# Kernel optimization log

Measured on AMD Instinct MI355X. Metric: run time of the kernel, lower is better.

The kernel has to match this reference:

```python
import jax, jax.numpy as jnp
import numpy as np

N_NODES = 50000
N_EDGES = 800000
LATENT = 32
NODE_IN = 6
EDGE_IN = 3
STEPS = 10
OUT_DIM = 1
NEG_SLOPE = 0.01
LN_EPS = 1e-5


def _leaky(x):
    return jnp.where(x >= 0, x, NEG_SLOPE * x)


def _layernorm(x, scale, bias):
    mu = jnp.mean(x, axis=-1, keepdims=True)
    var = jnp.mean(jnp.square(x - mu), axis=-1, keepdims=True)
    return (x - mu) * jax.lax.rsqrt(var + LN_EPS) * scale + bias


def setup_inputs() -> dict:
    key = jax.random.key(0)
    ks = jax.random.split(key, 24)
    g = lambda i, shape, fan_in: (jax.random.normal(ks[i], shape, jnp.float32)
                                  / np.sqrt(fan_in)).astype(jnp.float32)
    return {
        "x": jax.random.normal(ks[0], (N_NODES, NODE_IN), jnp.float32),
        "edge_attr": jax.random.normal(ks[1], (N_EDGES, EDGE_IN), jnp.float32),
        "senders": jax.random.randint(ks[2], (N_EDGES,), 0, N_NODES, jnp.int32),
        "receivers": jax.random.randint(ks[3], (N_EDGES,), 0, N_NODES, jnp.int32),
        # input embedders (Linear + LeakyReLU)
        "node_enc_W": g(4, (NODE_IN, LATENT), NODE_IN),
        "node_enc_b": jnp.zeros((LATENT,), jnp.float32),
        "edge_enc_W": g(5, (EDGE_IN, LATENT), EDGE_IN),
        "edge_enc_b": jnp.zeros((LATENT,), jnp.float32),
        # per-step edge update: concat(e, x_src, x_dst) -> latent
        "edge_W": g(6, (STEPS, 3 * LATENT, LATENT), 3 * LATENT),
        "edge_b": jnp.zeros((STEPS, LATENT), jnp.float32),
        "edge_ln_scale": jnp.ones((STEPS, LATENT), jnp.float32),
        "edge_ln_bias": jnp.zeros((STEPS, LATENT), jnp.float32),
        # per-step node update: concat(x, agg) -> latent
        "node_W": g(7, (STEPS, 2 * LATENT, LATENT), 2 * LATENT),
        "node_b": jnp.zeros((STEPS, LATENT), jnp.float32),
        "node_ln_scale": jnp.ones((STEPS, LATENT), jnp.float32),
        "node_ln_bias": jnp.zeros((STEPS, LATENT), jnp.float32),
        # decoder
        "dec_W1": g(8, (LATENT, LATENT), LATENT),
        "dec_b1": jnp.zeros((LATENT,), jnp.float32),
        "dec_W2": g(9, (LATENT, OUT_DIM), LATENT),
        "dec_b2": jnp.zeros((OUT_DIM,), jnp.float32),
    }


def _forward(x, edge_attr, senders, receivers,
             node_enc_W, node_enc_b, edge_enc_W, edge_enc_b,
             edge_W, edge_b, edge_ln_scale, edge_ln_bias,
             node_W, node_b, node_ln_scale, node_ln_bias,
             dec_W1, dec_b1, dec_W2, dec_b2):
    n = x.shape[0]
    # encode raw features into latent space
    h = _leaky(x @ node_enc_W + node_enc_b)            # [N, L]
    e = _leaky(edge_attr @ edge_enc_W + edge_enc_b)    # [E, L]
    # receiver in-degree for scatter-mean (constant across steps)
    cnt = jax.ops.segment_sum(jnp.ones((e.shape[0],), e.dtype), receivers,
                              num_segments=n)
    inv_cnt = (1.0 / jnp.maximum(cnt, 1.0))[:, None]   # [N, 1]

    def step(carry, p):
        h, e = carry
        eW, eb, es, ebi, nW, nb, ns, nbi = p
        # edge update: MLP(concat(e, h_src, h_dst)) + inner LN + residual
        m = jnp.concatenate([e, h[senders], h[receivers]], axis=-1)  # [E, 3L]
        m = _layernorm(_leaky(m @ eW + eb), es, ebi)
        e = e + m
        # node update: scatter-mean over receivers, MLP + inner LN + residual
        agg = jax.ops.segment_sum(e, receivers, num_segments=n) * inv_cnt
        u = jnp.concatenate([h, agg], axis=-1)                       # [N, 2L]
        u = _layernorm(_leaky(u @ nW + nb), ns, nbi)
        h = h + u
        return (h, e), None

    (h, e), _ = jax.lax.scan(step, (h, e),
                             (edge_W, edge_b, edge_ln_scale, edge_ln_bias,
                              node_W, node_b, node_ln_scale, node_ln_bias))
    # decoder: Linear -> LeakyReLU -> Linear
    return _leaky(h @ dec_W1 + dec_b1) @ dec_W2 + dec_b2  # [N, 1]


def reference(x, edge_attr, senders, receivers,
              node_enc_W, node_enc_b, edge_enc_W, edge_enc_b,
              edge_W, edge_b, edge_ln_scale, edge_ln_bias,
              node_W, node_b, node_ln_scale, node_ln_bias,
              dec_W1, dec_b1, dec_W2, dec_b2):
    return _forward(x, edge_attr, senders, receivers,
                    node_enc_W, node_enc_b, edge_enc_W, edge_enc_b,
                    edge_W, edge_b, edge_ln_scale, edge_ln_bias,
                    node_W, node_b, node_ln_scale, node_ln_bias,
                    dec_W1, dec_b1, dec_W2, dec_b2)
```

## Files before the change

kernel.cpp:

```cpp
#include <hip/hip_runtime.h>
#include <hip/hip_bf16.h>

#define N_NODES 50000
#define N_EDGES 800000
#define LATENT 32
#define STEPS 10
#define NEG_SLOPE 0.01f
#define LN_EPS 1e-5f
#define N_TILES (N_EDGES / 16)
#define TPW 4
#define TILES_PER_BLOCK 16
#define SCAN_BLK 256
#define SCAN_NBLK ((N_NODES + SCAN_BLK - 1) / SCAN_BLK)
#define STG_STRIDE 36

typedef __attribute__((ext_vector_type(8))) __bf16 bf16x8;
typedef __attribute__((ext_vector_type(4))) __bf16 bf16x4;
typedef __attribute__((ext_vector_type(4))) float f32x4;

__device__ __forceinline__ float leaky(float x) {
    return x >= 0.0f ? x : NEG_SLOPE * x;
}

__device__ __forceinline__ float4 f4fma(float a, float4 b, float4 c) {
    c.x += a * b.x; c.y += a * b.y; c.z += a * b.z; c.w += a * b.w;
    return c;
}

__device__ __forceinline__ bf16x4 pack4(float4 v) {
    bf16x4 o;
    o[0] = (__bf16)v.x; o[1] = (__bf16)v.y; o[2] = (__bf16)v.z; o[3] = (__bf16)v.w;
    return o;
}


__global__ void encode_nodes_kernel(const float* __restrict__ x,
                                    const float* __restrict__ W,
                                    const float* __restrict__ b,
                                    float* __restrict__ h,
                                    __bf16* __restrict__ hbf) {
    __shared__ __align__(16) float Ws[6 * 32];
    __shared__ __align__(16) float bs[32];
    int tid = threadIdx.x;
    if (tid < 192) Ws[tid] = W[tid];
    if (tid < 32) bs[tid] = b[tid];
    __syncthreads();
    int n = blockIdx.x * blockDim.x + tid;
    if (n >= N_NODES) return;
    float xv[6];
#pragma unroll
    for (int k = 0; k < 6; k++) xv[k] = x[(size_t)n * 6 + k];
    float4 acc[8];
#pragma unroll
    for (int q = 0; q < 8; q++) acc[q] = *(const float4*)&bs[q * 4];
#pragma unroll
    for (int k = 0; k < 6; k++) {
#pragma unroll
        for (int q = 0; q < 8; q++) {
            float4 w = *(const float4*)&Ws[k * 32 + q * 4];
            acc[q] = f4fma(xv[k], w, acc[q]);
        }
    }
#pragma unroll
    for (int q = 0; q < 8; q++) {
        float4 o = acc[q];
        o.x = leaky(o.x); o.y = leaky(o.y); o.z = leaky(o.z); o.w = leaky(o.w);
        *(float4*)&h[(size_t)n * 32 + q * 4] = o;
        *(bf16x4*)&hbf[(size_t)n * 32 + q * 4] = pack4(o);
    }
}


__global__ void count_kernel(const int* __restrict__ recv, int* __restrict__ cnt) {
    int i = blockIdx.x * blockDim.x + threadIdx.x;
    if (i < N_EDGES) atomicAdd(&cnt[recv[i]], 1);
}

__global__ void csr_reduce_kernel(const int* __restrict__ cnt, int* __restrict__ partial) {
    __shared__ int sdata[SCAN_BLK];
    int tid = threadIdx.x;
    int idx = blockIdx.x * SCAN_BLK + tid;
    sdata[tid] = (idx < N_NODES) ? cnt[idx] : 0;
    __syncthreads();
#pragma unroll
    for (int off = SCAN_BLK / 2; off > 0; off >>= 1) {
        if (tid < off) sdata[tid] += sdata[tid + off];
        __syncthreads();
    }
    if (tid == 0) partial[blockIdx.x] = sdata[0];
}

__global__ void csr_scan_partials_kernel(int* __restrict__ partial,
                                         int* __restrict__ row_start) {
    __shared__ int sdata[SCAN_BLK];
    int tid = threadIdx.x;
    int v = (tid < SCAN_NBLK) ? partial[tid] : 0;
    sdata[tid] = v;
    __syncthreads();
#pragma unroll
    for (int off = 1; off < SCAN_BLK; off <<= 1) {
        int t = (tid >= off) ? sdata[tid - off] : 0;
        __syncthreads();
        sdata[tid] += t;
        __syncthreads();
    }
    if (tid < SCAN_NBLK) partial[tid] = sdata[tid] - v;
    if (tid == SCAN_BLK - 1) row_start[N_NODES] = sdata[SCAN_BLK - 1];
}

__global__ void csr_apply_kernel(const int* __restrict__ cnt,
                                 const int* __restrict__ partial,
                                 int* __restrict__ row_start,
                                 int* __restrict__ cursor) {
    __shared__ int sdata[SCAN_BLK];
    int tid = threadIdx.x;
    int idx = blockIdx.x * SCAN_BLK + tid;
    int v = (idx < N_NODES) ? cnt[idx] : 0;
    sdata[tid] = v;
    __syncthreads();
#pragma unroll
    for (int off = 1; off < SCAN_BLK; off <<= 1) {
        int t = (tid >= off) ? sdata[tid - off] : 0;
        __syncthreads();
        sdata[tid] += t;
        __syncthreads();
    }
    if (idx < N_NODES) {
        int out = partial[blockIdx.x] + sdata[tid] - v;
        row_start[idx] = out;
        cursor[idx] = out;
    }
}

__global__ void scatter_encode_kernel(const float* __restrict__ ea,
                                      const int* __restrict__ senders,
                                      const int* __restrict__ receivers,
                                      int* __restrict__ cursor,
                                      const float* __restrict__ W,
                                      const float* __restrict__ b,
                                      __bf16* __restrict__ e,
                                      unsigned int* __restrict__ sr_p) {
    __shared__ __align__(16) float Ws[3 * 32];
    __shared__ __align__(16) float bs[32];
    int tid = threadIdx.x;
    if (tid < 96) Ws[tid] = W[tid];
    if (tid < 32) bs[tid] = b[tid];
    __syncthreads();
    int i = blockIdx.x * blockDim.x + tid;
    if (i >= N_EDGES) return;
    int s = senders[i];
    int r = receivers[i];
    float xv[3];
#pragma unroll
    for (int k = 0; k < 3; k++) xv[k] = ea[(size_t)i * 3 + k];
    int pos = atomicAdd(&cursor[r], 1);
    float4 acc[8];
#pragma unroll
    for (int q = 0; q < 8; q++) acc[q] = *(const float4*)&bs[q * 4];
#pragma unroll
    for (int k = 0; k < 3; k++) {
#pragma unroll
        for (int q = 0; q < 8; q++) {
            float4 w = *(const float4*)&Ws[k * 32 + q * 4];
            acc[q] = f4fma(xv[k], w, acc[q]);
        }
    }
    __bf16* er = e + (size_t)pos * 32;
#pragma unroll
    for (int q = 0; q < 4; q++) {
        float4 lo = acc[2 * q], hi = acc[2 * q + 1];
        bf16x8 v;
        v[0] = (__bf16)leaky(lo.x); v[1] = (__bf16)leaky(lo.y);
        v[2] = (__bf16)leaky(lo.z); v[3] = (__bf16)leaky(lo.w);
        v[4] = (__bf16)leaky(hi.x); v[5] = (__bf16)leaky(hi.y);
        v[6] = (__bf16)leaky(hi.z); v[7] = (__bf16)leaky(hi.w);
        *(bf16x8*)(er + q * 8) = v;
    }
    sr_p[pos] = (unsigned int)s | ((unsigned int)r << 16);
}


__global__ __launch_bounds__(256) void edge_mfma_kernel(
    __bf16* __restrict__ e,
    const __bf16* __restrict__ hbf,
    const unsigned int* __restrict__ srp,
    const float* __restrict__ W,
    const float* __restrict__ bias,
    const float* __restrict__ ln_s,
    const float* __restrict__ ln_b) {
    __shared__ __align__(16) float stg[4][16 * STG_STRIDE];
    int tid = threadIdx.x;

    const int wave = tid >> 6;
    const int lane = tid & 63;
    const int n_ = lane & 15;
    const int quad = lane >> 4;
    const int rr = lane >> 2;
    const int jj = lane & 3;

    bf16x8 bf[3][2];
#pragma unroll
    for (int kc = 0; kc < 3; kc++)
#pragma unroll
        for (int oh = 0; oh < 2; oh++) {
            bf16x8 f;
#pragma unroll
            for (int j = 0; j < 8; j++)
                f[j] = (__bf16)W[(kc * 32 + quad * 8 + j) * 32 + oh * 16 + n_];
            bf[kc][oh] = f;
        }
    float bia0 = bias[n_], bia1 = bias[16 + n_];
    float lns8[8], lnb8[8];
    {
        f32x4 sa = *(const f32x4*)&ln_s[jj * 8];
        f32x4 sb = *(const f32x4*)&ln_s[jj * 8 + 4];
        f32x4 ba = *(const f32x4*)&ln_b[jj * 8];
        f32x4 bb = *(const f32x4*)&ln_b[jj * 8 + 4];
#pragma unroll
        for (int i = 0; i < 4; i++) {
            lns8[i] = sa[i]; lns8[4 + i] = sb[i];
            lnb8[i] = ba[i]; lnb8[4 + i] = bb[i];
        }
    }

    int tile0 = blockIdx.x * TILES_PER_BLOCK + wave * TPW;
    int ntiles = min(TPW, N_TILES - tile0);
    if (ntiles <= 0) return;
    float* mystg = stg[wave];
    const int ed0 = tile0 * 16 + n_;

    unsigned int sr0 = srp[ed0];
    bf16x8 aE = *(const bf16x8*)&e[(size_t)ed0 * 32 + quad * 8];
    bf16x8 aS = *(const bf16x8*)&hbf[(size_t)(sr0 & 0xFFFFu) * 32 + quad * 8];
    bf16x8 aR = *(const bf16x8*)&hbf[(size_t)(sr0 >> 16) * 32 + quad * 8];
    bf16x8 old = *(const bf16x8*)&e[(size_t)(tile0 * 16 + rr) * 32 + jj * 8];
    unsigned int sr_n = 0;
    if (ntiles > 1) sr_n = srp[ed0 + 16];

    for (int t = 0; t < ntiles; t++) {
        int e0 = (tile0 + t) * 16;

        f32x4 acc[2] = {{0.f, 0.f, 0.f, 0.f}, {0.f, 0.f, 0.f, 0.f}};
#pragma unroll
        for (int oh = 0; oh < 2; oh++) {
            acc[oh] = __builtin_amdgcn_mfma_f32_16x16x32_bf16(aE, bf[0][oh], acc[oh], 0, 0, 0);
            acc[oh] = __builtin_amdgcn_mfma_f32_16x16x32_bf16(aS, bf[1][oh], acc[oh], 0, 0, 0);
            acc[oh] = __builtin_amdgcn_mfma_f32_16x16x32_bf16(aR, bf[2][oh], acc[oh], 0, 0, 0);
        }

        bf16x8 aE_n = aE, aS_n = aS, aR_n = aR, old_n = old;
        if (t + 1 < ntiles) {
            int edn = ed0 + (t + 1) * 16;
            aE_n = *(const bf16x8*)&e[(size_t)edn * 32 + quad * 8];
            aS_n = *(const bf16x8*)&hbf[(size_t)(sr_n & 0xFFFFu) * 32 + quad * 8];
            aR_n = *(const bf16x8*)&hbf[(size_t)(sr_n >> 16) * 32 + quad * 8];
            old_n = *(const bf16x8*)&e[(size_t)(e0 + 16 + rr) * 32 + jj * 8];
            if (t + 2 < ntiles) sr_n = srp[ed0 + (t + 2) * 16];
        }

#pragma unroll
        for (int oh = 0; oh < 2; oh++)
#pragma unroll
            for (int g = 0; g < 4; g++)
                mystg[(quad * 4 + g) * STG_STRIDE + oh * 16 + n_] =
                    leaky(acc[oh][g] + (oh ? bia1 : bia0));
        __builtin_amdgcn_wave_barrier();

        f32x4 va = *(const f32x4*)&mystg[rr * STG_STRIDE + jj * 8];
        f32x4 vb = *(const f32x4*)&mystg[rr * STG_STRIDE + jj * 8 + 4];
        float s1 = va[0] + va[1] + va[2] + va[3] + vb[0] + vb[1] + vb[2] + vb[3];
        float s2 = va[0]*va[0] + va[1]*va[1] + va[2]*va[2] + va[3]*va[3]
                 + vb[0]*vb[0] + vb[1]*vb[1] + vb[2]*vb[2] + vb[3]*vb[3];
        s1 += __shfl_xor(s1, 1);  s2 += __shfl_xor(s2, 1);
        s1 += __shfl_xor(s1, 2);  s2 += __shfl_xor(s2, 2);
        float mu = s1 * (1.0f / 32.0f);
        float var = s2 * (1.0f / 32.0f) - mu * mu;
        float inv = rsqrtf(fmaxf(var, 0.0f) + LN_EPS);

        float v[8] = {va[0], va[1], va[2], va[3], vb[0], vb[1], vb[2], vb[3]};
        bf16x8 outp;
#pragma unroll
        for (int i = 0; i < 8; i++)
            outp[i] = (__bf16)((float)old[i] + (v[i] - mu) * inv * lns8[i] + lnb8[i]);
        *(bf16x8*)&e[(size_t)(e0 + rr) * 32 + jj * 8] = outp;
        __builtin_amdgcn_wave_barrier();

        aE = aE_n; aS = aS_n; aR = aR_n; old = old_n;
    }
}


__global__ __launch_bounds__(256, 1) void node_kernel(
                            float* __restrict__ h,
                            __bf16* __restrict__ hbf,
                            const __bf16* __restrict__ e,
                            const int* __restrict__ row_start,
                            const float* __restrict__ W,
                            const float* __restrict__ bias,
                            const float* __restrict__ ln_s,
                            const float* __restrict__ ln_b) {
    __shared__ __align__(16) float Ws[64 * 32];
    __shared__ __align__(16) float prm[96];
    int tid = threadIdx.x;
    {
        const float4* Wg = (const float4*)W;
        float4* Wl = (float4*)Ws;
#pragma unroll
        for (int r = 0; r < 2; r++) Wl[tid + r * 256] = Wg[tid + r * 256];
        if (tid < 32) {
            prm[tid] = bias[tid];
            prm[32 + tid] = ln_s[tid];
            prm[64 + tid] = ln_b[tid];
        }
    }
    __syncthreads();
    int n = blockIdx.x * blockDim.x + tid;
    if (n >= N_NODES) return;

    int beg = row_start[n], end = row_start[n + 1];
    float c[64];
#pragma unroll
    for (int q = 0; q < 8; q++) {
        float4 v = *(const float4*)&h[(size_t)n * 32 + q * 4];
        c[q * 4 + 0] = v.x; c[q * 4 + 1] = v.y; c[q * 4 + 2] = v.z; c[q * 4 + 3] = v.w;
    }
    float s[32];
#pragma unroll
    for (int k = 0; k < 32; k++) s[k] = 0.0f;

    int j = beg;
    for (; j + 3 < end; j += 4) {
        bf16x8 v[16];
#pragma unroll
        for (int r = 0; r < 4; r++) {
            const __bf16* er = e + (size_t)(j + r) * 32;
#pragma unroll
            for (int q = 0; q < 4; q++) v[r * 4 + q] = *(const bf16x8*)(er + q * 8);
        }
#pragma unroll
        for (int r = 0; r < 4; r++)
#pragma unroll
            for (int q = 0; q < 4; q++)
#pragma unroll
                for (int k = 0; k < 8; k++)
                    s[q * 8 + k] += (float)v[r * 4 + q][k];
    }
    for (; j < end; j++) {
        const __bf16* er = e + (size_t)j * 32;
#pragma unroll
        for (int q = 0; q < 4; q++) {
            bf16x8 v = *(const bf16x8*)(er + q * 8);
#pragma unroll
            for (int k = 0; k < 8; k++) s[q * 8 + k] += (float)v[k];
        }
    }
    float ic = 1.0f / fmaxf((float)(end - beg), 1.0f);
#pragma unroll
    for (int k = 0; k < 32; k++) c[32 + k] = s[k] * ic;

    float4 acc[8];
#pragma unroll
    for (int q = 0; q < 8; q++) acc[q] = *(const float4*)&prm[q * 4];
#pragma unroll
    for (int k = 0; k < 64; k++) {
#pragma unroll
        for (int q = 0; q < 8; q++) {
            float4 w = *(const float4*)&Ws[k * 32 + q * 4];
            acc[q] = f4fma(c[k], w, acc[q]);
        }
    }
    float m[32];
#pragma unroll
    for (int q = 0; q < 8; q++) {
        m[q * 4 + 0] = leaky(acc[q].x);
        m[q * 4 + 1] = leaky(acc[q].y);
        m[q * 4 + 2] = leaky(acc[q].z);
        m[q * 4 + 3] = leaky(acc[q].w);
    }
    float s1 = 0.0f, s2 = 0.0f;
#pragma unroll
    for (int i = 0; i < 32; i++) { s1 += m[i]; s2 += m[i] * m[i]; }
    float mu = s1 * (1.0f / 32.0f);
    float var = s2 * (1.0f / 32.0f) - mu * mu;
    float inv = rsqrtf(fmaxf(var, 0.0f) + LN_EPS);
#pragma unroll
    for (int q = 0; q < 8; q++) {
        float4 sc = *(const float4*)&prm[32 + q * 4];
        float4 bi = *(const float4*)&prm[64 + q * 4];
        float4 res;
        res.x = c[q * 4 + 0] + (m[q * 4 + 0] - mu) * inv * sc.x + bi.x;
        res.y = c[q * 4 + 1] + (m[q * 4 + 1] - mu) * inv * sc.y + bi.y;
        res.z = c[q * 4 + 2] + (m[q * 4 + 2] - mu) * inv * sc.z + bi.z;
        res.w = c[q * 4 + 3] + (m[q * 4 + 3] - mu) * inv * sc.w + bi.w;
        *(float4*)&h[(size_t)n * 32 + q * 4] = res;
        *(bf16x4*)&hbf[(size_t)n * 32 + q * 4] = pack4(res);
    }
}


__global__ void decoder_kernel(const float* __restrict__ h,
                               const float* __restrict__ W1,
                               const float* __restrict__ b1,
                               const float* __restrict__ W2,
                               const float* __restrict__ b2,
                               float* __restrict__ out) {
    __shared__ __align__(16) float W1s[32 * 32];
    __shared__ __align__(16) float prm[65];
    int tid = threadIdx.x;
    {
        const float4* Wg = (const float4*)W1;
        float4* Wl = (float4*)W1s;
        Wl[tid] = Wg[tid];
        if (tid < 32) { prm[tid] = b1[tid]; prm[32 + tid] = W2[tid]; }
        if (tid == 0) prm[64] = b2[0];
    }
    __syncthreads();
    int n = blockIdx.x * blockDim.x + tid;
    if (n >= N_NODES) return;
    float hv[32];
#pragma unroll
    for (int q = 0; q < 8; q++) {
        float4 v = *(const float4*)&h[(size_t)n * 32 + q * 4];
        hv[q * 4 + 0] = v.x; hv[q * 4 + 1] = v.y; hv[q * 4 + 2] = v.z; hv[q * 4 + 3] = v.w;
    }
    float4 acc[8];
#pragma unroll
    for (int q = 0; q < 8; q++) acc[q] = *(const float4*)&prm[q * 4];
#pragma unroll
    for (int k = 0; k < 32; k++) {
#pragma unroll
        for (int q = 0; q < 8; q++) {
            float4 w = *(const float4*)&W1s[k * 32 + q * 4];
            acc[q] = f4fma(hv[k], w, acc[q]);
        }
    }
    float o = prm[64];
#pragma unroll
    for (int q = 0; q < 8; q++) {
        o += leaky(acc[q].x) * prm[32 + q * 4 + 0];
        o += leaky(acc[q].y) * prm[32 + q * 4 + 1];
        o += leaky(acc[q].z) * prm[32 + q * 4 + 2];
        o += leaky(acc[q].w) * prm[32 + q * 4 + 3];
    }
    out[n] = o;
}


extern "C" void kernel_launch(void* const* d_in, const int* in_sizes, int n_in,
                              void* d_out, int out_size, void* d_ws, size_t ws_size,
                              hipStream_t stream) {
    const float* x          = (const float*)d_in[0];
    const float* edge_attr  = (const float*)d_in[1];
    const int*   senders    = (const int*)d_in[2];
    const int*   receivers  = (const int*)d_in[3];
    const float* node_enc_W = (const float*)d_in[4];
    const float* node_enc_b = (const float*)d_in[5];
    const float* edge_enc_W = (const float*)d_in[6];
    const float* edge_enc_b = (const float*)d_in[7];
    const float* edge_W     = (const float*)d_in[8];
    const float* edge_b     = (const float*)d_in[9];
    const float* edge_ln_s  = (const float*)d_in[10];
    const float* edge_ln_b  = (const float*)d_in[11];
    const float* node_W     = (const float*)d_in[12];
    const float* node_b     = (const float*)d_in[13];
    const float* node_ln_s  = (const float*)d_in[14];
    const float* node_ln_b  = (const float*)d_in[15];
    const float* dec_W1     = (const float*)d_in[16];
    const float* dec_b1     = (const float*)d_in[17];
    const float* dec_W2     = (const float*)d_in[18];
    const float* dec_b2     = (const float*)d_in[19];
    float* out = (float*)d_out;

    char* ws = (char*)d_ws;
    size_t off = 0;
    auto alloc = [&](size_t bytes) -> void* {
        void* p = ws + off;
        off = (off + bytes + 255) & ~(size_t)255;
        return p;
    };
    float*        h         = (float*)alloc((size_t)N_NODES * 32 * 4);
    __bf16*       hbf       = (__bf16*)alloc((size_t)N_NODES * 32 * 2);
    __bf16*       e         = (__bf16*)alloc((size_t)N_EDGES * 32 * 2);
    int*          cnt       = (int*)alloc((size_t)N_NODES * 4);
    int*          row_start = (int*)alloc((size_t)(N_NODES + 1) * 4);
    int*          cursor    = (int*)alloc((size_t)N_NODES * 4);
    unsigned int* sr_p      = (unsigned int*)alloc((size_t)N_EDGES * 4);
    int*          partial   = (int*)alloc((size_t)SCAN_BLK * 4);
    (void)ws_size; (void)in_sizes; (void)n_in; (void)out_size;

    hipMemsetAsync(cnt, 0, (size_t)N_NODES * 4, stream);
    encode_nodes_kernel<<<(N_NODES + 255) / 256, 256, 0, stream>>>(x, node_enc_W, node_enc_b, h, hbf);
    count_kernel<<<(N_EDGES + 255) / 256, 256, 0, stream>>>(receivers, cnt);
    csr_reduce_kernel<<<SCAN_NBLK, SCAN_BLK, 0, stream>>>(cnt, partial);
    csr_scan_partials_kernel<<<1, SCAN_BLK, 0, stream>>>(partial, row_start);
    csr_apply_kernel<<<SCAN_NBLK, SCAN_BLK, 0, stream>>>(cnt, partial, row_start, cursor);
    scatter_encode_kernel<<<(N_EDGES + 255) / 256, 256, 0, stream>>>(
        edge_attr, senders, receivers, cursor, edge_enc_W, edge_enc_b, e, sr_p);

    int edge_blocks = (N_TILES + TILES_PER_BLOCK - 1) / TILES_PER_BLOCK;
    for (int s = 0; s < STEPS; s++) {
        edge_mfma_kernel<<<edge_blocks, 256, 0, stream>>>(
            e, hbf, sr_p,
            edge_W + (size_t)s * 96 * 32, edge_b + s * 32,
            edge_ln_s + s * 32, edge_ln_b + s * 32);
        node_kernel<<<(N_NODES + 255) / 256, 256, 0, stream>>>(
            h, hbf, e, row_start, node_W + (size_t)s * 64 * 32, node_b + s * 32,
            node_ln_s + s * 32, node_ln_b + s * 32);
    }
    decoder_kernel<<<(N_NODES + 255) / 256, 256, 0, stream>>>(h, dec_W1, dec_b1, dec_W2, dec_b2, out);
}
```

Before: 681.7 us.

## Fuse edge and node updates into one per-step kernel over receiver-sorted node blocks

Each message-passing step now runs as one kernel instead of separate edge and node kernels. A block owns 64 consecutive nodes and their contiguous receiver-sorted edge range, computes the edge MFMA update for those edges, then after a block barrier aggregates them and applies the node MLP with four threads per node. Node state is double-buffered so other blocks can still read the previous step's hbf while h is overwritten. This removes a launch per step and lets the node pass read freshly written edges while they are likely still in cache, but blocks now get uneven edge counts and partial 16-edge tiles, and the larger shared-memory footprint may lower occupancy.

Measured after the change: 709.6 us. +4.1%, slower.

```diff
diff --git a/kernel.cpp b/kernel.cpp
--- a/kernel.cpp
+++ b/kernel.cpp
@@ -7,12 +7,12 @@
 #define STEPS 10
 #define NEG_SLOPE 0.01f
 #define LN_EPS 1e-5f
-#define N_TILES (N_EDGES / 16)
-#define TPW 4
-#define TILES_PER_BLOCK 16
 #define SCAN_BLK 256
 #define SCAN_NBLK ((N_NODES + SCAN_BLK - 1) / SCAN_BLK)
 #define STG_STRIDE 36
+#define NODES_PER_BLOCK 64
+#define STEP_BLOCKS ((N_NODES + NODES_PER_BLOCK - 1) / NODES_PER_BLOCK)
+#define CPAD 65
 
 typedef __attribute__((ext_vector_type(8))) __bf16 bf16x8;
 typedef __attribute__((ext_vector_type(4))) __bf16 bf16x4;
@@ -180,17 +180,28 @@
 }
 
 
-__global__ __launch_bounds__(256) void edge_mfma_kernel(
+__global__ __launch_bounds__(256) void fused_step_kernel(
     __bf16* __restrict__ e,
-    const __bf16* __restrict__ hbf,
+    const __bf16* __restrict__ hbf_in,
+    __bf16* __restrict__ hbf_out,
+    const float* __restrict__ h_in,
+    float* __restrict__ h_out,
     const unsigned int* __restrict__ srp,
-    const float* __restrict__ W,
-    const float* __restrict__ bias,
-    const float* __restrict__ ln_s,
-    const float* __restrict__ ln_b) {
+    const int* __restrict__ row_start,
+    const float* __restrict__ eW,
+    const float* __restrict__ eb,
+    const float* __restrict__ els,
+    const float* __restrict__ elb,
+    const float* __restrict__ nW,
+    const float* __restrict__ nb,
+    const float* __restrict__ nls,
+    const float* __restrict__ nlb) {
     __shared__ __align__(16) float stg[4][16 * STG_STRIDE];
-    int tid = threadIdx.x;
-
+    __shared__ __align__(16) float Ws[64 * 32];
+    __shared__ __align__(16) float cL[NODES_PER_BLOCK * CPAD];
+    __shared__ __align__(16) float prm[96];
+
+    int tid = threadIdx.x;
     const int wave = tid >> 6;
     const int lane = tid & 63;
     const int n_ = lane & 15;
@@ -198,7 +209,19 @@
     const int rr = lane >> 2;
     const int jj = lane & 3;
 
-    bf16x8 bf[3][2];
+    {
+        const float4* Wg = (const float4*)nW;
+        float4* Wl = (float4*)Ws;
+        Wl[tid] = Wg[tid];
+        Wl[tid + 256] = Wg[tid + 256];
+        if (tid < 32) {
+            prm[tid] = nb[tid];
+            prm[32 + tid] = nls[tid];
+            prm[64 + tid] = nlb[tid];
+        }
+    }
+
+    bf16x8 bfr[3][2];
 #pragma unroll
     for (int kc = 0; kc < 3; kc++)
 #pragma unroll
@@ -206,16 +229,16 @@
             bf16x8 f;
 #pragma unroll
             for (int j = 0; j < 8; j++)
-                f[j] = (__bf16)W[(kc * 32 + quad * 8 + j) * 32 + oh * 16 + n_];
-            bf[kc][oh] = f;
-        }
-    float bia0 = bias[n_], bia1 = bias[16 + n_];
+                f[j] = (__bf16)eW[(kc * 32 + quad * 8 + j) * 32 + oh * 16 + n_];
+            bfr[kc][oh] = f;
+        }
+    float bia0 = eb[n_], bia1 = eb[16 + n_];
     float lns8[8], lnb8[8];
     {
-        f32x4 sa = *(const f32x4*)&ln_s[jj * 8];
-        f32x4 sb = *(const f32x4*)&ln_s[jj * 8 + 4];
-        f32x4 ba = *(const f32x4*)&ln_b[jj * 8];
-        f32x4 bb = *(const f32x4*)&ln_b[jj * 8 + 4];
+        f32x4 sa = *(const f32x4*)&els[jj * 8];
+        f32x4 sb = *(const f32x4*)&els[jj * 8 + 4];
+        f32x4 ba = *(const f32x4*)&elb[jj * 8];
+        f32x4 bb = *(const f32x4*)&elb[jj * 8 + 4];
 #pragma unroll
         for (int i = 0; i < 4; i++) {
             lns8[i] = sa[i]; lns8[4 + i] = sb[i];
@@ -223,39 +246,47 @@
         }
     }
 
-    int tile0 = blockIdx.x * TILES_PER_BLOCK + wave * TPW;
-    int ntiles = min(TPW, N_TILES - tile0);
-    if (ntiles <= 0) return;
+    const int n0 = blockIdx.x * NODES_PER_BLOCK;
+    const int nn = min(NODES_PER_BLOCK, N_NODES - n0);
+    const int beg = row_start[n0];
+    const int end = row_start[n0 + nn];
+    const int nt = (end - beg + 15) >> 4;
     float* mystg = stg[wave];
-    const int ed0 = tile0 * 16 + n_;
-
-    unsigned int sr0 = srp[ed0];
-    bf16x8 aE = *(const bf16x8*)&e[(size_t)ed0 * 32 + quad * 8];
-    bf16x8 aS = *(const bf16x8*)&hbf[(size_t)(sr0 & 0xFFFFu) * 32 + quad * 8];
-    bf16x8 aR = *(const bf16x8*)&hbf[(size_t)(sr0 >> 16) * 32 + quad * 8];
-    bf16x8 old = *(const bf16x8*)&e[(size_t)(tile0 * 16 + rr) * 32 + jj * 8];
-    unsigned int sr_n = 0;
-    if (ntiles > 1) sr_n = srp[ed0 + 16];
-
-    for (int t = 0; t < ntiles; t++) {
-        int e0 = (tile0 + t) * 16;
+
+    unsigned int sr_n2 = 0;
+    bf16x8 aE{}, aS{}, aR{}, old{};
+    if (wave < nt) {
+        int jb = beg + wave * 16;
+        int ja = min(jb + n_, N_EDGES - 1);
+        unsigned int sr_c = srp[ja];
+        aE  = *(const bf16x8*)&e[(size_t)ja * 32 + quad * 8];
+        aS  = *(const bf16x8*)&hbf_in[(size_t)(sr_c & 0xFFFFu) * 32 + quad * 8];
+        aR  = *(const bf16x8*)&hbf_in[(size_t)(sr_c >> 16) * 32 + quad * 8];
+        old = *(const bf16x8*)&e[(size_t)min(jb + rr, N_EDGES - 1) * 32 + jj * 8];
+        if (wave + 4 < nt)
+            sr_n2 = srp[min(beg + (wave + 4) * 16 + n_, N_EDGES - 1)];
+    }
+    for (int t = wave; t < nt; t += 4) {
+        int e0 = beg + t * 16;
 
         f32x4 acc[2] = {{0.f, 0.f, 0.f, 0.f}, {0.f, 0.f, 0.f, 0.f}};
 #pragma unroll
         for (int oh = 0; oh < 2; oh++) {
-            acc[oh] = __builtin_amdgcn_mfma_f32_16x16x32_bf16(aE, bf[0][oh], acc[oh], 0, 0, 0);
-            acc[oh] = __builtin_amdgcn_mfma_f32_16x16x32_bf16(aS, bf[1][oh], acc[oh], 0, 0, 0);
-            acc[oh] = __builtin_amdgcn_mfma_f32_16x16x32_bf16(aR, bf[2][oh], acc[oh], 0, 0, 0);
+            acc[oh] = __builtin_amdgcn_mfma_f32_16x16x32_bf16(aE, bfr[0][oh], acc[oh], 0, 0, 0);
+            acc[oh] = __builtin_amdgcn_mfma_f32_16x16x32_bf16(aS, bfr[1][oh], acc[oh], 0, 0, 0);
+            acc[oh] = __builtin_amdgcn_mfma_f32_16x16x32_bf16(aR, bfr[2][oh], acc[oh], 0, 0, 0);
         }
 
         bf16x8 aE_n = aE, aS_n = aS, aR_n = aR, old_n = old;
-        if (t + 1 < ntiles) {
-            int edn = ed0 + (t + 1) * 16;
-            aE_n = *(const bf16x8*)&e[(size_t)edn * 32 + quad * 8];
-            aS_n = *(const bf16x8*)&hbf[(size_t)(sr_n & 0xFFFFu) * 32 + quad * 8];
-            aR_n = *(const bf16x8*)&hbf[(size_t)(sr_n >> 16) * 32 + quad * 8];
-            old_n = *(const bf16x8*)&e[(size_t)(e0 + 16 + rr) * 32 + jj * 8];
-            if (t + 2 < ntiles) sr_n = srp[ed0 + (t + 2) * 16];
+        if (t + 4 < nt) {
+            int jb = beg + (t + 4) * 16;
+            int ja = min(jb + n_, N_EDGES - 1);
+            aE_n  = *(const bf16x8*)&e[(size_t)ja * 32 + quad * 8];
+            aS_n  = *(const bf16x8*)&hbf_in[(size_t)(sr_n2 & 0xFFFFu) * 32 + quad * 8];
+            aR_n  = *(const bf16x8*)&hbf_in[(size_t)(sr_n2 >> 16) * 32 + quad * 8];
+            old_n = *(const bf16x8*)&e[(size_t)min(jb + rr, N_EDGES - 1) * 32 + jj * 8];
+            if (t + 8 < nt)
+                sr_n2 = srp[min(beg + (t + 8) * 16 + n_, N_EDGES - 1)];
         }
 
 #pragma unroll
@@ -282,118 +313,85 @@
 #pragma unroll
         for (int i = 0; i < 8; i++)
             outp[i] = (__bf16)((float)old[i] + (v[i] - mu) * inv * lns8[i] + lnb8[i]);
-        *(bf16x8*)&e[(size_t)(e0 + rr) * 32 + jj * 8] = outp;
+        if (e0 + rr < end)
+            *(bf16x8*)&e[(size_t)(e0 + rr) * 32 + jj * 8] = outp;
         __builtin_amdgcn_wave_barrier();
 
         aE = aE_n; aS = aS_n; aR = aR_n; old = old_n;
     }
-}
-
-
-__global__ __launch_bounds__(256, 1) void node_kernel(
-                            float* __restrict__ h,
-                            __bf16* __restrict__ hbf,
-                            const __bf16* __restrict__ e,
-                            const int* __restrict__ row_start,
-                            const float* __restrict__ W,
-                            const float* __restrict__ bias,
-                            const float* __restrict__ ln_s,
-                            const float* __restrict__ ln_b) {
-    __shared__ __align__(16) float Ws[64 * 32];
-    __shared__ __align__(16) float prm[96];
-    int tid = threadIdx.x;
-    {
-        const float4* Wg = (const float4*)W;
-        float4* Wl = (float4*)Ws;
-#pragma unroll
-        for (int r = 0; r < 2; r++) Wl[tid + r * 256] = Wg[tid + r * 256];
-        if (tid < 32) {
-            prm[tid] = bias[tid];
-            prm[32 + tid] = ln_s[tid];
-            prm[64 + tid] = ln_b[tid];
-        }
-    }
-    __syncthreads();
-    int n = blockIdx.x * blockDim.x + tid;
-    if (n >= N_NODES) return;
-
-    int beg = row_start[n], end = row_start[n + 1];
-    float c[64];
-#pragma unroll
-    for (int q = 0; q < 8; q++) {
-        float4 v = *(const float4*)&h[(size_t)n * 32 + q * 4];
-        c[q * 4 + 0] = v.x; c[q * 4 + 1] = v.y; c[q * 4 + 2] = v.z; c[q * 4 + 3] = v.w;
-    }
-    float s[32];
-#pragma unroll
-    for (int k = 0; k < 32; k++) s[k] = 0.0f;
-
-    int j = beg;
-    for (; j + 3 < end; j += 4) {
-        bf16x8 v[16];
-#pragma unroll
-        for (int r = 0; r < 4; r++) {
-            const __bf16* er = e + (size_t)(j + r) * 32;
-#pragma unroll
-            for (int q = 0; q < 4; q++) v[r * 4 + q] = *(const bf16x8*)(er + q * 8);
-        }
-#pragma unroll
-        for (int r = 0; r < 4; r++)
-#pragma unroll
-            for (int q = 0; q < 4; q++)
-#pragma unroll
-                for (int k = 0; k < 8; k++)
-                    s[q * 8 + k] += (float)v[r * 4 + q][k];
-    }
-    for (; j < end; j++) {
-        const __bf16* er = e + (size_t)j * 32;
-#pragma unroll
-        for (int q = 0; q < 4; q++) {
-            bf16x8 v = *(const bf16x8*)(er + q * 8);
-#pragma unroll
-            for (int k = 0; k < 8; k++) s[q * 8 + k] += (float)v[k];
-        }
-    }
-    float ic = 1.0f / fmaxf((float)(end - beg), 1.0f);
-#pragma unroll
-    for (int k = 0; k < 32; k++) c[32 + k] = s[k] * ic;
-
-    float4 acc[8];
-#pragma unroll
-    for (int q = 0; q < 8; q++) acc[q] = *(const float4*)&prm[q * 4];
-#pragma unroll
-    for (int k = 0; k < 64; k++) {
-#pragma unroll
-        for (int q = 0; q < 8; q++) {
-            float4 w = *(const float4*)&Ws[k * 32 + q * 4];
-            acc[q] = f4fma(c[k], w, acc[q]);
-        }
-    }
-    float m[32];
-#pragma unroll
-    for (int q = 0; q < 8; q++) {
-        m[q * 4 + 0] = leaky(acc[q].x);
-        m[q * 4 + 1] = leaky(acc[q].y);
-        m[q * 4 + 2] = leaky(acc[q].z);
-        m[q * 4 + 3] = leaky(acc[q].w);
-    }
-    float s1 = 0.0f, s2 = 0.0f;
-#pragma unroll
-    for (int i = 0; i < 32; i++) { s1 += m[i]; s2 += m[i] * m[i]; }
-    float mu = s1 * (1.0f / 32.0f);
-    float var = s2 * (1.0f / 32.0f) - mu * mu;
-    float inv = rsqrtf(fmaxf(var, 0.0f) + LN_EPS);
-#pragma unroll
-    for (int q = 0; q < 8; q++) {
-        float4 sc = *(const float4*)&prm[32 + q * 4];
-        float4 bi = *(const float4*)&prm[64 + q * 4];
-        float4 res;
-        res.x = c[q * 4 + 0] + (m[q * 4 + 0] - mu) * inv * sc.x + bi.x;
-        res.y = c[q * 4 + 1] + (m[q * 4 + 1] - mu) * inv * sc.y + bi.y;
-        res.z = c[q * 4 + 2] + (m[q * 4 + 2] - mu) * inv * sc.z + bi.z;
-        res.w = c[q * 4 + 3] + (m[q * 4 + 3] - mu) * inv * sc.w + bi.w;
-        *(float4*)&h[(size_t)n * 32 + q * 4] = res;
-        *(bf16x4*)&hbf[(size_t)n * 32 + q * 4] = pack4(res);
+
+    __syncthreads();
+
+    const int nl = tid >> 2;
+    const int cq = tid & 3;
+    float hreg[8] = {0, 0, 0, 0, 0, 0, 0, 0};
+    if (nl < nn) {
+        int n = n0 + nl;
+        int bn = row_start[n], en = row_start[n + 1];
+        float s8[8];
+#pragma unroll
+        for (int k = 0; k < 8; k++) s8[k] = 0.f;
+        int j = bn;
+        for (; j + 3 < en; j += 4) {
+            bf16x8 v0 = *(const bf16x8*)&e[(size_t)j * 32 + cq * 8];
+            bf16x8 v1 = *(const bf16x8*)&e[(size_t)(j + 1) * 32 + cq * 8];
+            bf16x8 v2 = *(const bf16x8*)&e[(size_t)(j + 2) * 32 + cq * 8];
+            bf16x8 v3 = *(const bf16x8*)&e[(size_t)(j + 3) * 32 + cq * 8];
+#pragma unroll
+            for (int k = 0; k < 8; k++)
+                s8[k] += (float)v0[k] + (float)v1[k] + (float)v2[k] + (float)v3[k];
+        }
+        for (; j < en; j++) {
+            bf16x8 v = *(const bf16x8*)&e[(size_t)j * 32 + cq * 8];
+#pragma unroll
+            for (int k = 0; k < 8; k++) s8[k] += (float)v[k];
+        }
+        float ic = 1.0f / fmaxf((float)(en - bn), 1.0f);
+        float4 hv0 = *(const float4*)&h_in[(size_t)n * 32 + cq * 8];
+        float4 hv1 = *(const float4*)&h_in[(size_t)n * 32 + cq * 8 + 4];
+        hreg[0] = hv0.x; hreg[1] = hv0.y; hreg[2] = hv0.z; hreg[3] = hv0.w;
+        hreg[4] = hv1.x; hreg[5] = hv1.y; hreg[6] = hv1.z; hreg[7] = hv1.w;
+        float* crow = &cL[nl * CPAD];
+#pragma unroll
+        for (int k = 0; k < 8; k++) {
+            crow[cq * 8 + k] = hreg[k];
+            crow[32 + cq * 8 + k] = s8[k] * ic;
+        }
+    }
+    __syncthreads();
+    if (nl < nn) {
+        int n = n0 + nl;
+        float4 acc0 = *(const float4*)&prm[cq * 8];
+        float4 acc1 = *(const float4*)&prm[cq * 8 + 4];
+        const float* crow = &cL[nl * CPAD];
+#pragma unroll
+        for (int k = 0; k < 64; k++) {
+            float ck = crow[k];
+            acc0 = f4fma(ck, *(const float4*)&Ws[k * 32 + cq * 8], acc0);
+            acc1 = f4fma(ck, *(const float4*)&Ws[k * 32 + cq * 8 + 4], acc1);
+        }
+        float m8[8] = {leaky(acc0.x), leaky(acc0.y), leaky(acc0.z), leaky(acc0.w),
+                       leaky(acc1.x), leaky(acc1.y), leaky(acc1.z), leaky(acc1.w)};
+        float s1 = 0.f, s2 = 0.f;
+#pragma unroll
+        for (int k = 0; k < 8; k++) { s1 += m8[k]; s2 += m8[k] * m8[k]; }
+        s1 += __shfl_xor(s1, 1);  s2 += __shfl_xor(s2, 1);
+        s1 += __shfl_xor(s1, 2);  s2 += __shfl_xor(s2, 2);
+        float mu = s1 * (1.0f / 32.0f);
+        float var = s2 * (1.0f / 32.0f) - mu * mu;
+        float inv = rsqrtf(fmaxf(var, 0.0f) + LN_EPS);
+        float res[8];
+#pragma unroll
+        for (int k = 0; k < 8; k++)
+            res[k] = hreg[k] + (m8[k] - mu) * inv * prm[32 + cq * 8 + k] + prm[64 + cq * 8 + k];
+        float4 r0 = {res[0], res[1], res[2], res[3]};
+        float4 r1 = {res[4], res[5], res[6], res[7]};
+        *(float4*)&h_out[(size_t)n * 32 + cq * 8] = r0;
+        *(float4*)&h_out[(size_t)n * 32 + cq * 8 + 4] = r1;
+        bf16x8 hb;
+#pragma unroll
+        for (int k = 0; k < 8; k++) hb[k] = (__bf16)res[k];
+        *(bf16x8*)&hbf_out[(size_t)n * 32 + cq * 8] = hb;
     }
 }
 
@@ -478,8 +476,10 @@
         off = (off + bytes + 255) & ~(size_t)255;
         return p;
     };
-    float*        h         = (float*)alloc((size_t)N_NODES * 32 * 4);
-    __bf16*       hbf       = (__bf16*)alloc((size_t)N_NODES * 32 * 2);
+    float*        h0        = (float*)alloc((size_t)N_NODES * 32 * 4);
+    float*        h1        = (float*)alloc((size_t)N_NODES * 32 * 4);
+    __bf16*       hbf0      = (__bf16*)alloc((size_t)N_NODES * 32 * 2);
+    __bf16*       hbf1      = (__bf16*)alloc((size_t)N_NODES * 32 * 2);
     __bf16*       e         = (__bf16*)alloc((size_t)N_EDGES * 32 * 2);
     int*          cnt       = (int*)alloc((size_t)N_NODES * 4);
     int*          row_start = (int*)alloc((size_t)(N_NODES + 1) * 4);
@@ -489,7 +489,7 @@
     (void)ws_size; (void)in_sizes; (void)n_in; (void)out_size;
 
     hipMemsetAsync(cnt, 0, (size_t)N_NODES * 4, stream);
-    encode_nodes_kernel<<<(N_NODES + 255) / 256, 256, 0, stream>>>(x, node_enc_W, node_enc_b, h, hbf);
+    encode_nodes_kernel<<<(N_NODES + 255) / 256, 256, 0, stream>>>(x, node_enc_W, node_enc_b, h0, hbf0);
     count_kernel<<<(N_EDGES + 255) / 256, 256, 0, stream>>>(receivers, cnt);
     csr_reduce_kernel<<<SCAN_NBLK, SCAN_BLK, 0, stream>>>(cnt, partial);
     csr_scan_partials_kernel<<<1, SCAN_BLK, 0, stream>>>(partial, row_start);
@@ -497,15 +497,17 @@
     scatter_encode_kernel<<<(N_EDGES + 255) / 256, 256, 0, stream>>>(
         edge_attr, senders, receivers, cursor, edge_enc_W, edge_enc_b, e, sr_p);
 
-    int edge_blocks = (N_TILES + TILES_PER_BLOCK - 1) / TILES_PER_BLOCK;
+    float*  hbufs[2]  = {h0, h1};
+    __bf16* hbbufs[2] = {hbf0, hbf1};
     for (int s = 0; s < STEPS; s++) {
-        edge_mfma_kernel<<<edge_blocks, 256, 0, stream>>>(
-            e, hbf, sr_p,
+        int in = s & 1, outb = 1 - in;
+        fused_step_kernel<<<STEP_BLOCKS, 256, 0, stream>>>(
+            e, hbbufs[in], hbbufs[outb], hbufs[in], hbufs[outb],
+            sr_p, row_start,
             edge_W + (size_t)s * 96 * 32, edge_b + s * 32,
-            edge_ln_s + s * 32, edge_ln_b + s * 32);
-        node_kernel<<<(N_NODES + 255) / 256, 256, 0, stream>>>(
-            h, hbf, e, row_start, node_W + (size_t)s * 64 * 32, node_b + s * 32,
+            edge_ln_s + s * 32, edge_ln_b + s * 32,
+            node_W + (size_t)s * 64 * 32, node_b + s * 32,
             node_ln_s + s * 32, node_ln_b + s * 32);
     }
-    decoder_kernel<<<(N_NODES + 255) / 256, 256, 0, stream>>>(h, dec_W1, dec_b1, dec_W2, dec_b2, out);
-}
+    decoder_kernel<<<(N_NODES + 255) / 256, 256, 0, stream>>>(h0, dec_W1, dec_b1, dec_W2, dec_b2, out);
+}
```
